# Performance work log

Measured on AMD Instinct MI355X. Metric: run time of the kernel, lower is better.

The kernel has to match this reference:

```python
import jax, jax.numpy as jnp
import numpy as np

C = 256      # embed_dim
GROUP = 2    # conv groups
K = 3        # kernel/pool size
K2 = K * K
OG = 8       # offset groups (hard-coded in Similarity_cal)
NEX = 3      # exemplars per image (out_conv expects group*3*4 channels)


def conv2d(x, w, b, pad):
    y = jax.lax.conv_general_dilated(x, w, (1, 1), [(pad, pad), (pad, pad)],
                                     dimension_numbers=("NCHW", "OIHW", "NCHW"))
    return y + b[None, :, None, None]


def ln_c(x, g, b, eps=1e-5):
    # LayerNorm over the channel axis of NCHW (torch permutes to NHWC, LN, permute back)
    mu = x.mean(axis=1, keepdims=True)
    var = ((x - mu) ** 2).mean(axis=1, keepdims=True)
    return (x - mu) / jnp.sqrt(var + eps) * g[None, :, None, None] + b[None, :, None, None]


def bilinear_gather(img, py, px):
    # img [Cg,H,W]; py,px [K2,H,W] -> samples [Cg,K2,H,W], zero outside borders
    Cg, H, W = img.shape
    y0f = jnp.floor(py); x0f = jnp.floor(px)
    wy = py - y0f; wx = px - x0f
    y0 = y0f.astype(jnp.int32); x0 = x0f.astype(jnp.int32)
    flat = img.reshape(Cg, H * W)

    def corner(yy, xx, w):
        valid = (yy >= 0) & (yy < H) & (xx >= 0) & (xx < W)
        idx = jnp.clip(yy, 0, H - 1) * W + jnp.clip(xx, 0, W - 1)
        v = jnp.take(flat, idx.reshape(-1), axis=1).reshape(Cg, K2, H, W)
        return v * (w * valid)[None]

    return (corner(y0, x0, (1 - wy) * (1 - wx)) + corner(y0, x0 + 1, (1 - wy) * wx)
            + corner(y0 + 1, x0, wy * (1 - wx)) + corner(y0 + 1, x0 + 1, wy * wx))


def deform_conv(x, offset, mask, weight, dilation):
    # x [C,H,W]; offset [2*OG*K2,H,W]; mask [OG*K2,H,W] (softmaxed); weight [NEX*GROUP, C//GROUP, K, K]
    Cc, H, W = x.shape
    pad = (K - 1) * dilation // 2
    off = offset.reshape(OG, K2, 2, H, W)  # (dy, dx) per offset-group / tap
    kk = jnp.arange(K, dtype=x.dtype)
    ky = jnp.repeat(kk, K) * dilation - pad  # [K2]
    kx = jnp.tile(kk, K) * dilation - pad
    ii = jnp.arange(H, dtype=x.dtype)
    jj = jnp.arange(W, dtype=x.dtype)
    py = ii[None, None, :, None] + ky[None, :, None, None] + off[:, :, 0]  # [OG,K2,H,W]
    px = jj[None, None, None, :] + kx[None, :, None, None] + off[:, :, 1]
    xg = x.reshape(OG, Cc // OG, H, W)
    samp = jax.vmap(bilinear_gather)(xg, py, px)              # [OG,Cg,K2,H,W]
    samp = samp * mask.reshape(OG, 1, K2, H, W)               # modulation
    samp = samp.reshape(GROUP, Cc // GROUP, K2, H, W)
    wR = weight.reshape(NEX * GROUP, Cc // GROUP, K2)
    gidx = jnp.arange(NEX * GROUP) // NEX                     # out-channel -> conv group
    return jnp.einsum("rck,rckhw->rhw", wR, samp[gidx])       # [NEX*GROUP,H,W]


def forward(querys_feat, supports_feat, in_w, in_b, ln_g, ln_b, out_w, out_b,
            offw1, offb1, mskw1, mskb1, offw2, offb2, mskw2, mskb2,
            offw4, offb4, mskw4, mskb4):
    B = querys_feat.shape[0]
    q = ln_c(conv2d(querys_feat, in_w, in_b, 0), ln_g, ln_b)                 # [B,C,H,W]
    s = supports_feat.reshape(B * NEX, C, K, K)
    s = ln_c(conv2d(s, in_w, in_b, 0), ln_g, ln_b).reshape(B, NEX, C, K, K)

    def offs(wo, bo, wm, bm):
        o = conv2d(q, wo, bo, (K - 1) // 2)
        m = jax.nn.softmax(conv2d(q, wm, bm, (K - 1) // 2), axis=1)  # softmax over all OG*K2 channels
        return o, m

    o1, m1 = offs(offw1, offb1, mskw1, mskb1)
    o2, m2 = offs(offw2, offb2, mskw2, mskb2)
    o4, m4 = offs(offw4, offb4, mskw4, mskb4)

    def per_sample(qi, si, o1i, m1i, o2i, m2i, o4i, m4i):
        w = si.reshape(NEX * GROUP, C // GROUP, K, K)         # dynamic per-exemplar kernels
        pooled = si.max(axis=(2, 3)).reshape(NEX * GROUP, C // GROUP)
        gidx = jnp.arange(NEX * GROUP) // NEX
        qg = qi.reshape(GROUP, C // GROUP, *qi.shape[1:])
        sim0 = jnp.einsum("rc,rchw->rhw", pooled, qg[gidx])   # grouped 1x1 conv branch
        d1 = deform_conv(qi, o1i, m1i, w, 1)
        d2 = deform_conv(qi, o2i, m2i, w, 2)
        d4 = deform_conv(qi, o4i, m4i, w, 4)
        return jnp.concatenate([sim0, d1, d2, d4], axis=0)    # [GROUP*3*4, H, W]

    sim = jax.vmap(per_sample)(q, s, o1, m1, o2, m2, o4, m4)
    return conv2d(sim, out_w, out_b, 0)                        # [B,C,H,W]


def setup_inputs() -> dict:
    key = jax.random.key(0)
    ks = jax.random.split(key, 20)
    B, H, W = 2, 96, 96
    inp = {
        "querys_feat": jax.random.normal(ks[0], (B, C, H, W), jnp.float32),
        "supports_feat": jax.random.normal(ks[1], (B, NEX, C, K, K), jnp.float32),
        "in_w": jax.random.normal(ks[2], (C, C, 1, 1), jnp.float32) / 16.0,
        "in_b": jax.random.normal(ks[3], (C,), jnp.float32) * 0.02,
        "ln_g": jnp.ones((C,), jnp.float32),
        "ln_b": jnp.zeros((C,), jnp.float32),
        "out_w": jax.random.normal(ks[4], (C, GROUP * 3 * 4, 1, 1), jnp.float32) * 0.2,
        "out_b": jax.random.normal(ks[5], (C,), jnp.float32) * 0.02,
    }
    i = 6
    for d in (1, 2, 4):
        inp[f"offw{d}"] = jax.random.normal(ks[i], (2 * OG * K2, C, K, K), jnp.float32) * 0.01; i += 1
        inp[f"offb{d}"] = jax.random.normal(ks[i], (2 * OG * K2,), jnp.float32) * 0.1; i += 1
        inp[f"mskw{d}"] = jax.random.normal(ks[i], (OG * K2, C, K, K), jnp.float32) * 0.02; i += 1
        inp[f"mskb{d}"] = jax.random.normal(ks[i], (OG * K2,), jnp.float32) * 0.1; i += 1
    return inp


def reference(querys_feat, supports_feat, in_w, in_b, ln_g, ln_b, out_w, out_b,
              offw1, offb1, mskw1, mskb1, offw2, offb2, mskw2, mskb2,
              offw4, offb4, mskw4, mskb4):
    return forward(querys_feat, supports_feat, in_w, in_b, ln_g, ln_b, out_w, out_b,
                   offw1, offb1, mskw1, mskb1, offw2, offb2, mskw2, mskb2,
                   offw4, offb4, mskw4, mskb4)
```

## Files before the change

### kernel.cpp

```cpp
#include <hip/hip_runtime.h>
#include <hip/hip_bf16.h>
#include <math.h>

#define HH 96
#define WWID 96
#define HW 9216
#define CC 256
#define BB 2
#define PROW 104
#define PCOL 128
#define PPX (PROW * PCOL)

typedef float f32x4 __attribute__((ext_vector_type(4)));
typedef _Float16 f16x8 __attribute__((ext_vector_type(8)));
typedef _Float16 h2v __attribute__((ext_vector_type(2)));

__device__ inline unsigned int pack2h(float a, float b) {
  unsigned short ua = __builtin_bit_cast(unsigned short, (_Float16)a);
  unsigned short ub = __builtin_bit_cast(unsigned short, (_Float16)b);
  return (unsigned int)ua | ((unsigned int)ub << 16);
}
__device__ inline float h_lo(unsigned int u) {
  return (float)__builtin_bit_cast(_Float16, (unsigned short)(u & 0xffffu));
}
__device__ inline float h_hi(unsigned int u) {
  return (float)__builtin_bit_cast(_Float16, (unsigned short)(u >> 16));
}

#if defined(__has_builtin)
#if __has_builtin(__builtin_amdgcn_fdot2)
#define FDOT2(a, b, c) __builtin_amdgcn_fdot2((a), (b), (c), false)
#endif
#endif
#ifndef FDOT2
#define FDOT2(a, b, c) ((c) + (float)(a).x * (float)(b).x + (float)(a).y * (float)(b).y)
#endif

__device__ inline void gload_lds16(const void* g, void* l) {
  __builtin_amdgcn_global_load_lds(
      (const __attribute__((address_space(1))) void*)g,
      (__attribute__((address_space(3))) void*)l, 16, 0, 0);
}

__global__ void k_transpose_w(const float* __restrict__ in_w, float* __restrict__ wT) {
  int k = blockIdx.x, c = threadIdx.x;
  wT[k * CC + c] = in_w[c * CC + k];
}

__global__ void k_packw(const float* __restrict__ ow1, const float* __restrict__ ob1,
                        const float* __restrict__ mw1, const float* __restrict__ mb1,
                        const float* __restrict__ ow2, const float* __restrict__ ob2,
                        const float* __restrict__ mw2, const float* __restrict__ mb2,
                        const float* __restrict__ ow4, const float* __restrict__ ob4,
                        const float* __restrict__ mw4, const float* __restrict__ mb4,
                        _Float16* __restrict__ Whf, float* __restrict__ Ball) {
  int idx = blockIdx.x * 256 + threadIdx.x;
  if (idx >= 3 * 256 * 2304) return;
  int d = idx / (256 * 2304);
  int rem = idx - d * 256 * 2304;
  int co = rem / 2304;
  int k = rem - co * 2304;
  int j = k >> 8, ci = k & 255;
  const float* ow = d == 0 ? ow1 : (d == 1 ? ow2 : ow4);
  const float* mw = d == 0 ? mw1 : (d == 1 ? mw2 : mw4);
  float v = 0.f;
  if (co < 144) v = ow[co * 2304 + ci * 9 + j];
  else if (co < 216) v = mw[(co - 144) * 2304 + ci * 9 + j];
  Whf[idx] = (_Float16)v;
  if (idx < 768) {
    int dd = idx >> 8, cc = idx & 255;
    const float* obv = dd == 0 ? ob1 : (dd == 1 ? ob2 : ob4);
    const float* mbv = dd == 0 ? mb1 : (dd == 1 ? mb2 : mb4);
    float bv = 0.f;
    if (cc < 144) bv = obv[cc];
    else if (cc < 216) bv = mbv[cc - 144];
    Ball[idx] = bv;
  }
}

__global__ void k_conv1_ln_q(const float* __restrict__ qin, const float* __restrict__ wT,
                             const float* __restrict__ in_b, const float* __restrict__ ln_g,
                             const float* __restrict__ ln_b, float* __restrict__ q_hwc,
                             _Float16* __restrict__ qpad) {
  int bx = blockIdx.x;
  int b = bx / 288;
  int hw0 = (bx % 288) * 32;
  int t = threadIdx.x;
  int lane = t & 63;
  int wv_id = t >> 6;
  __shared__ float xs[32 * 260];
  const float* qb = qin + (size_t)b * CC * HW;
  #pragma unroll
  for (int i = 0; i < 32; ++i) {
    int idx = t + i * 256;
    int p = idx & 31;
    int k = idx >> 5;
    xs[p * 260 + k] = qb[k * HW + hw0 + p];
  }
  __syncthreads();
  float acc[8][4];
  #pragma unroll
  for (int p = 0; p < 8; ++p) { acc[p][0]=0.f; acc[p][1]=0.f; acc[p][2]=0.f; acc[p][3]=0.f; }
  const float4* wT4 = (const float4*)wT;
  int p0 = wv_id * 8;
  for (int k = 0; k < 256; k += 4) {
    float4 w0 = wT4[(k + 0) * 64 + lane];
    float4 w1 = wT4[(k + 1) * 64 + lane];
    float4 w2 = wT4[(k + 2) * 64 + lane];
    float4 w3 = wT4[(k + 3) * 64 + lane];
    #pragma unroll
    for (int p = 0; p < 8; ++p) {
      float4 xv = *(const float4*)&xs[(p0 + p) * 260 + k];
      acc[p][0] += w0.x * xv.x + w1.x * xv.y + w2.x * xv.z + w3.x * xv.w;
      acc[p][1] += w0.y * xv.x + w1.y * xv.y + w2.y * xv.z + w3.y * xv.w;
      acc[p][2] += w0.z * xv.x + w1.z * xv.y + w2.z * xv.z + w3.z * xv.w;
      acc[p][3] += w0.w * xv.x + w1.w * xv.y + w2.w * xv.z + w3.w * xv.w;
    }
  }
  float4 bb = ((const float4*)in_b)[lane];
  float4 g4 = ((const float4*)ln_g)[lane];
  float4 b4 = ((const float4*)ln_b)[lane];
  #pragma unroll
  for (int p = 0; p < 8; ++p) {
    float y0 = acc[p][0] + bb.x, y1 = acc[p][1] + bb.y;
    float y2 = acc[p][2] + bb.z, y3 = acc[p][3] + bb.w;
    float s1 = y0 + y1 + y2 + y3;
    float s2 = y0*y0 + y1*y1 + y2*y2 + y3*y3;
    #pragma unroll
    for (int off = 32; off; off >>= 1) { s1 += __shfl_xor(s1, off); s2 += __shfl_xor(s2, off); }
    float mu = s1 * (1.f / 256.f);
    float rstd = rsqrtf(s2 * (1.f / 256.f) - mu * mu + 1e-5f);
    float4 o;
    o.x = (y0 - mu) * rstd * g4.x + b4.x;
    o.y = (y1 - mu) * rstd * g4.y + b4.y;
    o.z = (y2 - mu) * rstd * g4.z + b4.z;
    o.w = (y3 - mu) * rstd * g4.w + b4.w;
    int hw = hw0 + p0 + p;
    ((float4*)q_hwc)[((size_t)b * HW + hw) * 64 + lane] = o;
    int hh = hw / 96, ww = hw - hh * 96;
    int ppx = (hh + 4) * PCOL + ww + 4;
    struct alignas(8) h4 { _Float16 h[4]; };
    h4 oh;
    oh.h[0] = (_Float16)o.x; oh.h[1] = (_Float16)o.y;
    oh.h[2] = (_Float16)o.z; oh.h[3] = (_Float16)o.w;
    *(h4*)(qpad + ((size_t)b * PPX + ppx) * CC + lane * 4) = oh;
  }
}

__global__ void k_conv1_ln_s(const float* __restrict__ sup, const float* __restrict__ wT,
                             const float* __restrict__ in_b, const float* __restrict__ ln_g,
                             const float* __restrict__ ln_b, float* __restrict__ s_ln,
                             float* __restrict__ pooled) {
  int img = blockIdx.x;
  int t = threadIdx.x;
  __shared__ float xs[2304];
  __shared__ float red1[256], red2[256];
  #pragma unroll
  for (int p = 0; p < 9; ++p) xs[t * 9 + p] = sup[(size_t)img * 2304 + t * 9 + p];
  __syncthreads();
  float acc[9];
  #pragma unroll
  for (int p = 0; p < 9; ++p) acc[p] = 0.f;
  for (int k = 0; k < 256; ++k) {
    float wv = wT[k * CC + t];
    #pragma unroll
    for (int p = 0; p < 9; ++p) acc[p] += wv * xs[k * 9 + p];
  }
  float bias = in_b[t];
  #pragma unroll
  for (int p = 0; p < 9; ++p) acc[p] += bias;
  float g = ln_g[t], be = ln_b[t];
  float vals[9];
  #pragma unroll
  for (int p = 0; p < 9; ++p) {
    red1[t] = acc[p]; red2[t] = acc[p] * acc[p];
    __syncthreads();
    for (int s = 128; s > 0; s >>= 1) {
      if (t < s) { red1[t] += red1[t + s]; red2[t] += red2[t + s]; }
      __syncthreads();
    }
    float mu = red1[0] * (1.f / 256.f);
    float var = red2[0] * (1.f / 256.f) - mu * mu;
    float rstd = rsqrtf(var + 1e-5f);
    vals[p] = (acc[p] - mu) * rstd * g + be;
    __syncthreads();
  }
  #pragma unroll
  for (int p = 0; p < 9; ++p) s_ln[(size_t)img * 2304 + t * 9 + p] = vals[p];
  float mx = vals[0];
  #pragma unroll
  for (int p = 1; p < 9; ++p) mx = fmaxf(mx, vals[p]);
  int b = img / 3, e = img % 3;
  pooled[((size_t)b * 6 + e * 2 + (t >> 7)) * 128 + (t & 127)] = mx;
}


#define BAR() __builtin_amdgcn_s_barrier()
#define SCHEDB() __builtin_amdgcn_sched_barrier(0)
#define VMCNT(N) asm volatile("s_waitcnt vmcnt(" #N ")" ::: "memory")

#define MMA_ONE(M, N, S, QM, QN) \
  acc[(QM)*4+(M)][(QN)*2+(N)] = __builtin_amdgcn_mfma_f32_16x16x32_f16( \
      af[M][S], bf[(QN)*2+(N)][S], acc[(QM)*4+(M)][(QN)*2+(N)], 0, 0, 0);

#define MMA_Q(QM, QN) { \
  __builtin_amdgcn_s_setprio(1); \
  MMA_ONE(0,0,0,QM,QN) MMA_ONE(1,0,0,QM,QN) MMA_ONE(2,0,0,QM,QN) MMA_ONE(3,0,0,QM,QN) \
  MMA_ONE(0,1,0,QM,QN) MMA_ONE(1,1,0,QM,QN) MMA_ONE(2,1,0,QM,QN) MMA_ONE(3,1,0,QM,QN) \
  MMA_ONE(0,0,1,QM,QN) MMA_ONE(1,0,1,QM,QN) MMA_ONE(2,0,1,QM,QN) MMA_ONE(3,0,1,QM,QN) \
  MMA_ONE(0,1,1,QM,QN) MMA_ONE(1,1,1,QM,QN) MMA_ONE(2,1,1,QM,QN) MMA_ONE(3,1,1,QM,QN) \
  __builtin_amdgcn_s_setprio(0); }

#define LDA(BUF, QM) { \
  const char* p_ = smemB + (BUF) * 65536 + (wm * 128 + (QM) * 64 + l15) * 128; \
  af[0][0] = *(const f16x8*)(p_ + 0*2048 + rc0); af[0][1] = *(const f16x8*)(p_ + 0*2048 + rc1); \
  af[1][0] = *(const f16x8*)(p_ + 1*2048 + rc0); af[1][1] = *(const f16x8*)(p_ + 1*2048 + rc1); \
  af[2][0] = *(const f16x8*)(p_ + 2*2048 + rc0); af[2][1] = *(const f16x8*)(p_ + 2*2048 + rc1); \
  af[3][0] = *(const f16x8*)(p_ + 3*2048 + rc0); af[3][1] = *(const f16x8*)(p_ + 3*2048 + rc1); }

#define LDB(BUF, QN) { \
  const char* p_ = smemB + (BUF) * 65536 + 32768 + (wn * 64 + (QN) * 32 + l15) * 128; \
  bf[(QN)*2+0][0] = *(const f16x8*)(p_ + 0*2048 + rc0); bf[(QN)*2+0][1] = *(const f16x8*)(p_ + 0*2048 + rc1); \
  bf[(QN)*2+1][0] = *(const f16x8*)(p_ + 1*2048 + rc0); bf[(QN)*2+1][1] = *(const f16x8*)(p_ + 1*2048 + rc1); }

#define STAGEA(TILE, Q) { \
  gload_lds16(aBase + (size_t)((Q) * 64) * 2304 + (TILE) * 64, \
              smemB + ((TILE) & 1) * 65536 + (((Q) * 64 + wv * 8) * 128)); \
  gload_lds16(aBase + (size_t)(128 + (Q) * 64) * 2304 + (TILE) * 64, \
              smemB + ((TILE) & 1) * 65536 + ((128 + (Q) * 64 + wv * 8) * 128)); }

#define STAGEB(TILE, Q, PPX0, PPX1) { \
  int j_ = (TILE) >> 2; \
  int offp_ = (j_ / 3 - 1) * PCOL + (j_ % 3) - 1; \
  int cb_ = ((TILE) & 3) * 64; \
  int rs_ = (wv >> 2) * 64 + (Q) * 32 + (wv & 3) * 8; \
  gload_lds16(bBase + (size_t)((PPX0) + offp_) * CC + cb_, \
              smemB + ((TILE) & 1) * 65536 + 32768 + (rs_ * 128)); \
  gload_lds16(bBase + (size_t)((PPX1) + offp_) * CC + cb_, \
              smemB + ((TILE) & 1) * 65536 + 32768 + ((128 + rs_) * 128)); }

__global__ void __launch_bounds__(512) k_conv3_mfma8(
    const _Float16* __restrict__ qpad, const _Float16* __restrict__ Whf,
    float* __restrict__ offbuf, float* __restrict__ mskbuf) {
  int nb = blockIdx.x;
  int z = blockIdx.y;
  int d = z >> 1, b = z & 1;
  int t = threadIdx.x;
  int lane = t & 63, wv = t >> 6;
  int wm = wv >> 2, wn = wv & 3;
  int quad = lane >> 4, l15 = lane & 15;
  int l8 = lane >> 3, c7 = lane & 7;

  __shared__ _Float16 __attribute__((aligned(16))) smem[65536];
  char* smemB = (char*)smem;

  const _Float16* Wd = Whf + (size_t)d * 256 * 2304;
  const _Float16* qb = qpad + (size_t)b * PPX * CC;

  int scol = ((c7 ^ l8) << 3);
  int rc0 = ((quad ^ (l15 & 7)) << 4);
  int rc1 = (((4 | quad) ^ (l15 & 7)) << 4);

  const _Float16* aBase = Wd + (size_t)(wv * 8 + l8) * 2304 + scol;
  const _Float16* bBase = qb + scol;

  int ppx00, ppx01, ppx10, ppx11;
  {
    int rbase = (wv >> 2) * 64 + (wv & 3) * 8 + l8;
    int px, hh, ww;
    px = nb * 256 + rbase;             hh = px / 96; ww = px - hh * 96; ppx00 = (hh + 4) * PCOL + ww + 4;
    px = nb * 256 + 128 + rbase;       hh = px / 96; ww = px - hh * 96; ppx01 = (hh + 4) * PCOL + ww + 4;
    px = nb * 256 + 32 + rbase;        hh = px / 96; ww = px - hh * 96; ppx10 = (hh + 4) * PCOL + ww + 4;
    px = nb * 256 + 160 + rbase;       hh = px / 96; ww = px - hh * 96; ppx11 = (hh + 4) * PCOL + ww + 4;
  }

  f32x4 acc[8][4];
  #pragma unroll
  for (int i = 0; i < 8; ++i)
    #pragma unroll
    for (int j = 0; j < 4; ++j) acc[i][j] = (f32x4){0.f, 0.f, 0.f, 0.f};

  f16x8 af[4][2], bf[4][2];

  STAGEA(0, 0);
  STAGEB(0, 1, ppx10, ppx11);
  STAGEA(0, 1);
  STAGEB(0, 0, ppx00, ppx01);
  STAGEA(1, 0);
  STAGEB(1, 1, ppx10, ppx11);
  VMCNT(4);
  BAR();
  SCHEDB();

  #pragma unroll 1
  for (int ii = 0; ii < 17; ++ii) {
    int ta = 2 * ii + 1, tb = 2 * ii + 2, tc = 2 * ii + 3;
    LDA(0, 0) LDB(0, 0)
    STAGEA(ta, 1);
    BAR(); MMA_Q(0, 0); BAR();
    LDB(0, 1)
    STAGEB(ta, 0, ppx00, ppx01);
    BAR(); MMA_Q(0, 1); BAR();
    LDA(0, 1)
    STAGEA(tb, 0);
    BAR(); MMA_Q(1, 1); BAR();
    STAGEB(tb, 1, ppx10, ppx11);
    VMCNT(4);
    BAR(); SCHEDB(); MMA_Q(1, 0); BAR();
    LDA(1, 0) LDB(1, 0)
    STAGEA(tb, 1);
    BAR(); MMA_Q(0, 0); BAR();
    LDB(1, 1)
    STAGEB(tb, 0, ppx00, ppx01);
    BAR(); MMA_Q(0, 1); BAR();
    LDA(1, 1)
    STAGEA(tc, 0);
    BAR(); MMA_Q(1, 1); BAR();
    STAGEB(tc, 1, ppx10, ppx11);
    VMCNT(4);
    BAR(); SCHEDB(); MMA_Q(1, 0); BAR();
  }

  LDA(0, 0) LDB(0, 0)
  STAGEA(35, 1);
  BAR(); MMA_Q(0, 0); BAR();
  LDB(0, 1)
  STAGEB(35, 0, ppx00, ppx01);
  BAR(); MMA_Q(0, 1); BAR();
  LDA(0, 1)
  BAR(); MMA_Q(1, 1); BAR();
  VMCNT(0);
  BAR(); SCHEDB(); MMA_Q(1, 0); BAR();
  LDA(1, 0) LDB(1, 0)
  BAR(); MMA_Q(0, 0); BAR();
  LDB(1, 1)
  BAR(); MMA_Q(0, 1); BAR();
  LDA(1, 1)
  BAR(); MMA_Q(1, 1); BAR();
  MMA_Q(1, 0);

  float* obP = offbuf + (size_t)(d * BB + b) * 144 * HW;
  float* mkP = mskbuf + (size_t)(d * BB + b) * 72 * HW;
  #pragma unroll
  for (int mi = 0; mi < 8; ++mi) {
    int co = wm * 128 + mi * 16 + quad * 4;
    #pragma unroll
    for (int ni = 0; ni < 4; ++ni) {
      int px = nb * 256 + wn * 64 + ni * 16 + l15;
      f32x4 v = acc[mi][ni];
      #pragma unroll
      for (int r = 0; r < 4; ++r) {
        int c2 = co + r;
        if (c2 < 144) obP[(size_t)c2 * HW + px] = v[r];
        else if (c2 < 216) mkP[(size_t)(c2 - 144) * HW + px] = v[r];
      }
    }
  }
}

__global__ void k_taps(const float* __restrict__ offbuf, const float* __restrict__ mskbuf,
                       const float* __restrict__ Ball, unsigned int* __restrict__ taprec) {
  int t = threadIdx.x;
  int sub = t & 7, pxl = t >> 3;
  int bx = blockIdx.x;
  int z = bx / 288;
  int px = (bx - z * 288) * 32 + pxl;
  int d = z >> 1;
  const float* Bd = Ball + d * 256;
  const float* mp = mskbuf + (size_t)z * 72 * HW + px;
  float lg[9];
  float mx = -1e30f;
  #pragma unroll
  for (int j = 0; j < 9; ++j) {
    int tk = sub + 8 * j;
    lg[j] = mp[(size_t)tk * HW] + Bd[144 + tk];
    mx = fmaxf(mx, lg[j]);
  }
  mx = fmaxf(mx, __shfl_xor(mx, 1));
  mx = fmaxf(mx, __shfl_xor(mx, 2));
  mx = fmaxf(mx, __shfl_xor(mx, 4));
  float s = 0.f;
  #pragma unroll
  for (int j = 0; j < 9; ++j) s += __expf(lg[j] - mx);
  s += __shfl_xor(s, 1);
  s += __shfl_xor(s, 2);
  s += __shfl_xor(s, 4);
  float rinv = 1.f / s;
  int dil = 1 << (z >> 1);
  int h = px / WWID, w = px - h * WWID;
  const float* ob = offbuf + (size_t)z * 144 * HW + px;
  int k = sub;
  #pragma unroll
  for (int j = 0; j < 9; ++j) {
    int tk = sub + 8 * j;
    float dy = ob[(size_t)(tk * 2 + 0) * HW] + Bd[tk * 2 + 0];
    float dx = ob[(size_t)(tk * 2 + 1) * HW] + Bd[tk * 2 + 1];
    float m = __expf(lg[j] - mx) * rinv;
    float py = (float)(h + (k / 3) * dil - dil) + dy;
    float pxx = (float)(w + (k % 3) * dil - dil) + dx;
    float y0f = floorf(py), x0f = floorf(pxx);
    int y0 = (int)y0f, x0 = (int)x0f;
    float wy = py - y0f, wx = pxx - x0f;
    bool vy0 = (unsigned)y0 < 96u, vy1 = (unsigned)(y0 + 1) < 96u;
    bool vx0 = (unsigned)x0 < 96u, vx1 = (unsigned)(x0 + 1) < 96u;
    float w00 = (vy0 && vx0) ? (1.f - wy) * (1.f - wx) * m : 0.f;
    float w01 = (vy0 && vx1) ? (1.f - wy) * wx * m : 0.f;
    float w10 = (vy1 && vx0) ? wy * (1.f - wx) * m : 0.f;
    float w11 = (vy1 && vx1) ? wy * wx * m : 0.f;
    int iy = min(max(y0 + 4, 0), 102);
    int ix = min(max(x0 + 4, 0), 126);
    unsigned int* r = taprec + (((size_t)(z * 72 + tk)) * HW + px) * 3;
    r[0] = pack2h(w00, w01);
    r[1] = pack2h(w10, w11);
    r[2] = (unsigned int)(iy * PCOL + ix);
    k += 8; if (k >= 9) k -= 9;
  }
}

__global__ void k_sim0(const float* __restrict__ qt, const float* __restrict__ pooled,
                       float* __restrict__ sim) {
  int b = blockIdx.z, h = blockIdx.y, seg = blockIdx.x;
  int t = threadIdx.x;
  int pxl = t >> 5, lane = t & 31;
  int wcol = seg * 8 + pxl;
  int hw = h * WWID + wcol;
  __shared__ float plds[768];
  for (int i = t; i < 768; i += 256) plds[i] = pooled[(size_t)b * 768 + i];
  __syncthreads();
  const float* qtb = qt + (size_t)b * HW * CC;
  float acc[6] = {0.f, 0.f, 0.f, 0.f, 0.f, 0.f};
  #pragma unroll
  for (int m = 0; m < 8; ++m) {
    int cfull = m * 32 + lane;
    float qv = qtb[(size_t)hw * CC + cfull];
    if (m < 4) {
      int cp = cfull;
      acc[0] += plds[0 * 128 + cp] * qv;
      acc[1] += plds[1 * 128 + cp] * qv;
      acc[2] += plds[2 * 128 + cp] * qv;
    } else {
      int cp = cfull - 128;
      acc[3] += plds[3 * 128 + cp] * qv;
      acc[4] += plds[4 * 128 + cp] * qv;
      acc[5] += plds[5 * 128 + cp] * qv;
    }
  }
  #pragma unroll
  for (int r = 0; r < 6; ++r) {
    float v = acc[r];
    #pragma unroll
    for (int off = 16; off; off >>= 1) v += __shfl_down(v, off, 32);
    if (lane == 0) sim[((size_t)b * 24 + r) * HW + hw] = v;
  }
}

#define DO_P(U0, U1, IDX, P) { \
  h2v u0_ = __builtin_bit_cast(h2v, (U0)); \
  h2v u1_ = __builtin_bit_cast(h2v, (U1)); \
  const h2v* b0_ = qc + (size_t)(IDX) * 128; \
  h2v q00_ = b0_[0], q01_ = b0_[128]; \
  h2v q10_ = b0_[16384], q11_ = b0_[16384 + 128]; \
  h2v s_ = q00_ * (h2v){u0_.x, u0_.x} + q01_ * (h2v){u0_.y, u0_.y} \
         + q10_ * (h2v){u1_.x, u1_.x} + q11_ * (h2v){u1_.y, u1_.y}; \
  acc[P][0] = FDOT2(wr0, s_, acc[P][0]); \
  acc[P][1] = FDOT2(wr1, s_, acc[P][1]); \
  acc[P][2] = FDOT2(wr2, s_, acc[P][2]); }

__global__ void __launch_bounds__(256) k_deform(
    const _Float16* __restrict__ qpad, const unsigned int* __restrict__ taprec,
    const float* __restrict__ s_ln, float* __restrict__ sim) {
  int bid = blockIdx.x;
  int slab = bid & 7;
  int j = bid >> 3;
  int z = j / 72;
  int rem = j - z * 72;
  int yhalf = rem / 36;
  int segin = rem - yhalf * 36;
  int seg = slab * 36 + segin;
  int d_idx = z >> 1, b = z & 1;
  int t = threadIdx.x;
  int g = t >> 5, lane = t & 31;
  int half16 = lane >> 4, l16 = lane & 15;
  __shared__ _Float16 wh[9 * 384];
  __shared__ unsigned int rlds[36 * 96];
  int px0 = seg * 32;
  int tkbase = yhalf * 36;
  const unsigned int* tz = taprec + (size_t)z * 72 * HW * 3;
  for (int i2 = t; i2 < 3456; i2 += 256) {
    int c = i2 / 9, k = i2 % 9;
    wh[k * 384 + c] = (_Float16)s_ln[(size_t)b * 6912 + yhalf * 3456 + i2];
  }
  for (int i2 = t; i2 < 3456; i2 += 256) {
    int tko = i2 / 96, dw = i2 - tko * 96;
    rlds[i2] = tz[((size_t)(tkbase + tko) * HW + px0) * 3 + dw];
  }
  __syncthreads();
  int pg = g * 4;
  int pxb = px0 + pg;
  const unsigned int* whd = (const unsigned int*)wh;
  const _Float16* qb = qpad + (size_t)b * PPX * CC;

  float acc[4][3];
  #pragma unroll
  for (int p = 0; p < 4; ++p)
    #pragma unroll
    for (int r = 0; r < 3; ++r) acc[p][r] = 0.f;

  #pragma unroll 1
  for (int ogp = 0; ogp < 2; ++ogp) {
    int og = yhalf * 4 + ogp * 2 + half16;
    int qch = og * 32 + l16 * 2;
    int wcol = qch - yhalf * 128;
    int tko = (ogp * 2 + half16) * 9;
    const h2v* qc = (const h2v*)(qb + qch);
    #pragma unroll 3
    for (int k = 0; k < 9; ++k) {
      const unsigned int* rr = &rlds[(tko + k) * 96 + pg * 3];
      h2v wr0 = __builtin_bit_cast(h2v, whd[(k * 384 + 0 + wcol) >> 1]);
      h2v wr1 = __builtin_bit_cast(h2v, whd[(k * 384 + 128 + wcol) >> 1]);
      h2v wr2 = __builtin_bit_cast(h2v, whd[(k * 384 + 256 + wcol) >> 1]);
      DO_P(rr[0], rr[1], rr[2], 0)
      DO_P(rr[3], rr[4], rr[5], 1)
      DO_P(rr[6], rr[7], rr[8], 2)
      DO_P(rr[9], rr[10], rr[11], 3)
    }
  }

  #pragma unroll
  for (int p = 0; p < 4; ++p) {
    #pragma unroll
    for (int r = 0; r < 3; ++r) {
      float v = acc[p][r];
      #pragma unroll
      for (int off = 16; off; off >>= 1) v += __shfl_down(v, off, 32);
      if (lane == 0)
        sim[((size_t)b * 24 + 6 + 6 * d_idx + yhalf * 3 + r) * HW + pxb + p] = v;
    }
  }
}

__global__ void k_outconv(const float* __restrict__ sim, const float* __restrict__ out_w,
                          const float* __restrict__ out_b, float* __restrict__ out) {
  int hw = blockIdx.x * 256 + threadIdx.x;
  int co = blockIdx.y, b = blockIdx.z;
  const float* simb = sim + (size_t)b * 24 * HW;
  float a = out_b[co];
  #pragma unroll
  for (int r = 0; r < 24; ++r) a += out_w[co * 24 + r] * simb[(size_t)r * HW + hw];
  out[((size_t)b * CC + co) * HW + hw] = a;
}

extern "C" void kernel_launch(void* const* d_in, const int* in_sizes, int n_in,
                              void* d_out, int out_size, void* d_ws, size_t ws_size,
                              hipStream_t stream) {
  const float* querys = (const float*)d_in[0];
  const float* sup    = (const float*)d_in[1];
  const float* in_w   = (const float*)d_in[2];
  const float* in_b   = (const float*)d_in[3];
  const float* ln_g   = (const float*)d_in[4];
  const float* ln_b   = (const float*)d_in[5];
  const float* out_w  = (const float*)d_in[6];
  const float* out_b  = (const float*)d_in[7];
  const float* ow1 = (const float*)d_in[8];
  const float* ob1 = (const float*)d_in[9];
  const float* mw1 = (const float*)d_in[10];
  const float* mb1 = (const float*)d_in[11];
  const float* ow2 = (const float*)d_in[12];
  const float* ob2 = (const float*)d_in[13];
  const float* mw2 = (const float*)d_in[14];
  const float* mb2 = (const float*)d_in[15];
  const float* ow4 = (const float*)d_in[16];
  const float* ob4 = (const float*)d_in[17];
  const float* mw4 = (const float*)d_in[18];
  const float* mb4 = (const float*)d_in[19];
  float* out = (float*)d_out;

  float* ws_f   = (float*)d_ws;
  float* wT     = ws_f;
  _Float16* Whf = (_Float16*)(wT + 65536);
  float* Ball   = (float*)(Whf + 3 * 256 * 2304);
  float* q_hwc  = Ball + 1024;
  _Float16* qpad = (_Float16*)(q_hwc + (size_t)BB * HW * CC);
  float* s_ln   = (float*)(qpad + (size_t)BB * PPX * CC);
  float* pooled = s_ln + 13824;
  float* offbuf = pooled + 1536;
  float* mskbuf = offbuf + (size_t)3 * BB * 144 * HW;
  float* sim    = mskbuf + (size_t)3 * BB * 72 * HW;
  unsigned int* taprec = (unsigned int*)(sim + (size_t)BB * 24 * HW);

  hipMemsetAsync(qpad, 0, (size_t)BB * PPX * CC * sizeof(_Float16), stream);
  k_transpose_w<<<dim3(256), dim3(256), 0, stream>>>(in_w, wT);
  k_packw<<<dim3((3 * 256 * 2304 + 255) / 256), dim3(256), 0, stream>>>(
      ow1, ob1, mw1, mb1, ow2, ob2, mw2, mb2, ow4, ob4, mw4, mb4, Whf, Ball);
  k_conv1_ln_q<<<dim3(576), dim3(256), 0, stream>>>(querys, wT, in_b, ln_g, ln_b, q_hwc, qpad);
  k_conv1_ln_s<<<dim3(6), dim3(256), 0, stream>>>(sup, wT, in_b, ln_g, ln_b, s_ln, pooled);
  k_conv3_mfma8<<<dim3(36, 6), dim3(512), 0, stream>>>(qpad, Whf, offbuf, mskbuf);
  k_taps<<<dim3(1728), dim3(256), 0, stream>>>(offbuf, mskbuf, Ball, taprec);
  k_sim0<<<dim3(12, 96, BB), dim3(256), 0, stream>>>(q_hwc, pooled, sim);
  k_deform<<<dim3(3456), dim3(256), 0, stream>>>(qpad, taprec, s_ln, sim);
  k_outconv<<<dim3(36, 256, BB), dim3(256), 0, stream>>>(sim, out_w, out_b, out);
}
```

Baseline: 366.0 us.

## Fuse tap softmax and bilinear record generation into conv3 MFMA epilogue

The conv3 kernel no longer writes its offset and mask outputs to global fp32 buffers for a separate k_taps kernel. Its epilogue now stages the accumulators plus bias through shared memory in two halves, then computes the mask softmax, the bilinear weights and the indices, and writes the packed tap records directly. This removes a kernel launch and a round trip of roughly 6*216*9216 floats through global memory. In exchange it adds LDS staging, extra barriers and serial epilogue work inside a kernel that only has 216 blocks.

```diff
diff --git a/kernel.cpp b/kernel.cpp
--- a/kernel.cpp
+++ b/kernel.cpp
@@ -19,12 +19,6 @@
   unsigned short ua = __builtin_bit_cast(unsigned short, (_Float16)a);
   unsigned short ub = __builtin_bit_cast(unsigned short, (_Float16)b);
   return (unsigned int)ua | ((unsigned int)ub << 16);
-}
-__device__ inline float h_lo(unsigned int u) {
-  return (float)__builtin_bit_cast(_Float16, (unsigned short)(u & 0xffffu));
-}
-__device__ inline float h_hi(unsigned int u) {
-  return (float)__builtin_bit_cast(_Float16, (unsigned short)(u >> 16));
 }
 
 #if defined(__has_builtin)
@@ -241,7 +235,7 @@
 
 __global__ void __launch_bounds__(512) k_conv3_mfma8(
     const _Float16* __restrict__ qpad, const _Float16* __restrict__ Whf,
-    float* __restrict__ offbuf, float* __restrict__ mskbuf) {
+    const float* __restrict__ Ball, unsigned int* __restrict__ taprec) {
   int nb = blockIdx.x;
   int z = blockIdx.y;
   int d = z >> 1, b = z & 1;
@@ -339,81 +333,85 @@
   BAR(); MMA_Q(1, 1); BAR();
   MMA_Q(1, 0);
 
-  float* obP = offbuf + (size_t)(d * BB + b) * 144 * HW;
-  float* mkP = mskbuf + (size_t)(d * BB + b) * 72 * HW;
-  #pragma unroll
-  for (int mi = 0; mi < 8; ++mi) {
-    int co = wm * 128 + mi * 16 + quad * 4;
-    #pragma unroll
-    for (int ni = 0; ni < 4; ++ni) {
-      int px = nb * 256 + wn * 64 + ni * 16 + l15;
-      f32x4 v = acc[mi][ni];
+  BAR();
+  float* cs = (float*)smemB;
+  const float* Bd = Ball + d * 256;
+  unsigned int* tzo = taprec + (size_t)z * 72 * HW * 3;
+  int sub = t & 7;
+  int pxq = t >> 3;
+  int dil = 1 << d;
+
+  #pragma unroll 1
+  for (int H = 0; H < 2; ++H) {
+    if ((wn >> 1) == H) {
       #pragma unroll
-      for (int r = 0; r < 4; ++r) {
-        int c2 = co + r;
-        if (c2 < 144) obP[(size_t)c2 * HW + px] = v[r];
-        else if (c2 < 216) mkP[(size_t)(c2 - 144) * HW + px] = v[r];
+      for (int mi = 0; mi < 8; ++mi) {
+        int c2 = wm * 128 + mi * 16 + quad * 4;
+        if (c2 < 216) {
+          float4 bq = *(const float4*)(Bd + c2);
+          #pragma unroll
+          for (int ni = 0; ni < 4; ++ni) {
+            int pl = (wn & 1) * 64 + ni * 16 + l15;
+            f32x4 v = acc[mi][ni];
+            float* cp = &cs[pl * 225 + c2];
+            cp[0] = v[0] + bq.x; cp[1] = v[1] + bq.y;
+            cp[2] = v[2] + bq.z; cp[3] = v[3] + bq.w;
+          }
+        }
       }
     }
-  }
-}
-
-__global__ void k_taps(const float* __restrict__ offbuf, const float* __restrict__ mskbuf,
-                       const float* __restrict__ Ball, unsigned int* __restrict__ taprec) {
-  int t = threadIdx.x;
-  int sub = t & 7, pxl = t >> 3;
-  int bx = blockIdx.x;
-  int z = bx / 288;
-  int px = (bx - z * 288) * 32 + pxl;
-  int d = z >> 1;
-  const float* Bd = Ball + d * 256;
-  const float* mp = mskbuf + (size_t)z * 72 * HW + px;
-  float lg[9];
-  float mx = -1e30f;
-  #pragma unroll
-  for (int j = 0; j < 9; ++j) {
-    int tk = sub + 8 * j;
-    lg[j] = mp[(size_t)tk * HW] + Bd[144 + tk];
-    mx = fmaxf(mx, lg[j]);
-  }
-  mx = fmaxf(mx, __shfl_xor(mx, 1));
-  mx = fmaxf(mx, __shfl_xor(mx, 2));
-  mx = fmaxf(mx, __shfl_xor(mx, 4));
-  float s = 0.f;
-  #pragma unroll
-  for (int j = 0; j < 9; ++j) s += __expf(lg[j] - mx);
-  s += __shfl_xor(s, 1);
-  s += __shfl_xor(s, 2);
-  s += __shfl_xor(s, 4);
-  float rinv = 1.f / s;
-  int dil = 1 << (z >> 1);
-  int h = px / WWID, w = px - h * WWID;
-  const float* ob = offbuf + (size_t)z * 144 * HW + px;
-  int k = sub;
-  #pragma unroll
-  for (int j = 0; j < 9; ++j) {
-    int tk = sub + 8 * j;
-    float dy = ob[(size_t)(tk * 2 + 0) * HW] + Bd[tk * 2 + 0];
-    float dx = ob[(size_t)(tk * 2 + 1) * HW] + Bd[tk * 2 + 1];
-    float m = __expf(lg[j] - mx) * rinv;
-    float py = (float)(h + (k / 3) * dil - dil) + dy;
-    float pxx = (float)(w + (k % 3) * dil - dil) + dx;
-    float y0f = floorf(py), x0f = floorf(pxx);
-    int y0 = (int)y0f, x0 = (int)x0f;
-    float wy = py - y0f, wx = pxx - x0f;
-    bool vy0 = (unsigned)y0 < 96u, vy1 = (unsigned)(y0 + 1) < 96u;
-    bool vx0 = (unsigned)x0 < 96u, vx1 = (unsigned)(x0 + 1) < 96u;
-    float w00 = (vy0 && vx0) ? (1.f - wy) * (1.f - wx) * m : 0.f;
-    float w01 = (vy0 && vx1) ? (1.f - wy) * wx * m : 0.f;
-    float w10 = (vy1 && vx0) ? wy * (1.f - wx) * m : 0.f;
-    float w11 = (vy1 && vx1) ? wy * wx * m : 0.f;
-    int iy = min(max(y0 + 4, 0), 102);
-    int ix = min(max(x0 + 4, 0), 126);
-    unsigned int* r = taprec + (((size_t)(z * 72 + tk)) * HW + px) * 3;
-    r[0] = pack2h(w00, w01);
-    r[1] = pack2h(w10, w11);
-    r[2] = (unsigned int)(iy * PCOL + ix);
-    k += 8; if (k >= 9) k -= 9;
+    BAR();
+    #pragma unroll 1
+    for (int p = 0; p < 2; ++p) {
+      int pl = p * 64 + pxq;
+      int px = nb * 256 + H * 128 + pl;
+      const float* cr = &cs[pl * 225];
+      float lg[9];
+      float mx = -1e30f;
+      #pragma unroll
+      for (int j = 0; j < 9; ++j) {
+        lg[j] = cr[144 + sub + 8 * j];
+        mx = fmaxf(mx, lg[j]);
+      }
+      mx = fmaxf(mx, __shfl_xor(mx, 1));
+      mx = fmaxf(mx, __shfl_xor(mx, 2));
+      mx = fmaxf(mx, __shfl_xor(mx, 4));
+      float s = 0.f;
+      #pragma unroll
+      for (int j = 0; j < 9; ++j) s += __expf(lg[j] - mx);
+      s += __shfl_xor(s, 1);
+      s += __shfl_xor(s, 2);
+      s += __shfl_xor(s, 4);
+      float rinv = 1.f / s;
+      int h = px / WWID, w = px - h * WWID;
+      int k = sub;
+      #pragma unroll
+      for (int j = 0; j < 9; ++j) {
+        int tk = sub + 8 * j;
+        float dy = cr[tk * 2 + 0];
+        float dx = cr[tk * 2 + 1];
+        float m = __expf(lg[j] - mx) * rinv;
+        float py = (float)(h + (k / 3) * dil - dil) + dy;
+        float pxx = (float)(w + (k % 3) * dil - dil) + dx;
+        float y0f = floorf(py), x0f = floorf(pxx);
+        int y0 = (int)y0f, x0 = (int)x0f;
+        float wy = py - y0f, wx = pxx - x0f;
+        bool vy0 = (unsigned)y0 < 96u, vy1 = (unsigned)(y0 + 1) < 96u;
+        bool vx0 = (unsigned)x0 < 96u, vx1 = (unsigned)(x0 + 1) < 96u;
+        float w00 = (vy0 && vx0) ? (1.f - wy) * (1.f - wx) * m : 0.f;
+        float w01 = (vy0 && vx1) ? (1.f - wy) * wx * m : 0.f;
+        float w10 = (vy1 && vx0) ? wy * (1.f - wx) * m : 0.f;
+        float w11 = (vy1 && vx1) ? wy * wx * m : 0.f;
+        int iy = min(max(y0 + 4, 0), 102);
+        int ix = min(max(x0 + 4, 0), 126);
+        unsigned int* r = tzo + ((size_t)tk * HW + px) * 3;
+        r[0] = pack2h(w00, w01);
+        r[1] = pack2h(w10, w11);
+        r[2] = (unsigned int)(iy * PCOL + ix);
+        k += 8; if (k >= 9) k -= 9;
+      }
+    }
+    BAR();
   }
 }
 
@@ -583,10 +581,8 @@
   _Float16* qpad = (_Float16*)(q_hwc + (size_t)BB * HW * CC);
   float* s_ln   = (float*)(qpad + (size_t)BB * PPX * CC);
   float* pooled = s_ln + 13824;
-  float* offbuf = pooled + 1536;
-  float* mskbuf = offbuf + (size_t)3 * BB * 144 * HW;
-  float* sim    = mskbuf + (size_t)3 * BB * 72 * HW;
-  unsigned int* taprec = (unsigned int*)(sim + (size_t)BB * 24 * HW);
+  unsigned int* taprec = (unsigned int*)(pooled + 1536);
+  float* sim    = (float*)(taprec + (size_t)6 * 72 * HW * 3);
 
   hipMemsetAsync(qpad, 0, (size_t)BB * PPX * CC * sizeof(_Float16), stream);
   k_transpose_w<<<dim3(256), dim3(256), 0, stream>>>(in_w, wT);
@@ -594,8 +590,7 @@
       ow1, ob1, mw1, mb1, ow2, ob2, mw2, mb2, ow4, ob4, mw4, mb4, Whf, Ball);
   k_conv1_ln_q<<<dim3(576), dim3(256), 0, stream>>>(querys, wT, in_b, ln_g, ln_b, q_hwc, qpad);
   k_conv1_ln_s<<<dim3(6), dim3(256), 0, stream>>>(sup, wT, in_b, ln_g, ln_b, s_ln, pooled);
-  k_conv3_mfma8<<<dim3(36, 6), dim3(512), 0, stream>>>(qpad, Whf, offbuf, mskbuf);
-  k_taps<<<dim3(1728), dim3(256), 0, stream>>>(offbuf, mskbuf, Ball, taprec);
+  k_conv3_mfma8<<<dim3(36, 6), dim3(512), 0, stream>>>(qpad, Whf, Ball, taprec);
   k_sim0<<<dim3(12, 96, BB), dim3(256), 0, stream>>>(q_hwc, pooled, sim);
   k_deform<<<dim3(3456), dim3(256), 0, stream>>>(qpad, taprec, s_ln, sim);
   k_outconv<<<dim3(36, 256, BB), dim3(256), 0, stream>>>(sim, out_w, out_b, out);
```

Result: faster. 351.0 us (-4.1%).
